# Performance work log

Measured on AMD Instinct MI355X. Metric: run time of the kernel, lower is better.

## Reference

```python
import jax, jax.numpy as jnp
import numpy as np

T, N, L = 512, 128, 256           # encoder steps, batch, decode steps
KV, VS = 128, 128                 # key_size, value_size
EMB, HID, VOC = 256, 512, 34


def _lstm_cell(x, h, c, W_ih, W_hh, b_ih, b_hh):
    # PyTorch LSTMCell gate order: i, f, g, o
    g = x @ W_ih.T + b_ih + h @ W_hh.T + b_hh
    i, f, gg, o = jnp.split(g, 4, axis=-1)
    c2 = jax.nn.sigmoid(f) * c + jax.nn.sigmoid(i) * jnp.tanh(gg)
    h2 = jax.nn.sigmoid(o) * jnp.tanh(c2)
    return h2, c2


def setup_inputs() -> dict:
    k = jax.random.key(0)
    ks = jax.random.split(k, 16)
    s = 0.05
    return {
        "key": jax.random.normal(ks[0], (T, N, KV), jnp.float32),
        "values": jax.random.normal(ks[1], (T, N, VS), jnp.float32),
        "lens": jax.random.randint(ks[2], (N,), 1, T + 1),
        "text": jax.random.randint(ks[3], (N, L), 0, VOC),
        "emb": jax.random.normal(ks[4], (VOC, EMB), jnp.float32) * s,
        "W_ih1": jax.random.normal(ks[5], (4 * HID, EMB + VS), jnp.float32) * s,
        "W_hh1": jax.random.normal(ks[6], (4 * HID, HID), jnp.float32) * s,
        "b_ih1": jnp.zeros((4 * HID,), jnp.float32),
        "b_hh1": jnp.zeros((4 * HID,), jnp.float32),
        "W_ih2": jax.random.normal(ks[7], (4 * KV, HID), jnp.float32) * s,
        "W_hh2": jax.random.normal(ks[8], (4 * KV, KV), jnp.float32) * s,
        "b_ih2": jnp.zeros((4 * KV,), jnp.float32),
        "b_hh2": jnp.zeros((4 * KV,), jnp.float32),
        "W_out": jax.random.normal(ks[9], (VOC, KV + VS), jnp.float32) * s,
        "b_out": jnp.zeros((VOC,), jnp.float32),
    }


def reference(key, values, lens, text, emb, W_ih1, W_hh1, b_ih1, b_hh1,
              W_ih2, W_hh2, b_ih2, b_hh2, W_out, b_out):
    # key/values: (T, N, 128); teacher-forced decode over L steps.
    pad_mask = jnp.arange(T)[None, :] >= lens[:, None]        # (N, T)
    embs = emb[text]                                          # (N, L, EMB)
    embs = jnp.transpose(embs, (1, 0, 2))                     # (L, N, EMB)

    def step(carry, e_t):
        h1, c1, h2, c2, ctx = carry
        x = jnp.concatenate([e_t, ctx], axis=-1)
        h1, c1 = _lstm_cell(x, h1, c1, W_ih1, W_hh1, b_ih1, b_hh1)
        h2, c2 = _lstm_cell(h1, h2, c2, W_ih2, W_hh2, b_ih2, b_hh2)
        # masked bmm attention: energy (N, T)
        energy = jnp.einsum('tnk,nk->nt', key, h2)
        energy = jnp.where(pad_mask, -1e9, energy)
        attn = jax.nn.softmax(energy, axis=1)
        ctx = jnp.einsum('nt,tnv->nv', attn, values)
        pred = jnp.concatenate([h2, ctx], axis=-1) @ W_out.T + b_out
        return (h1, c1, h2, c2, ctx), pred

    init = (jnp.zeros((N, HID)), jnp.zeros((N, HID)),
            jnp.zeros((N, KV)), jnp.zeros((N, KV)),
            jnp.zeros((N, VS)))
    _, preds = jax.lax.scan(step, init, embs)                 # (L, N, VOC)
    return jnp.transpose(preds, (1, 0, 2))                    # (N, L, VOC)
```

## Files before the change

kernel.cpp:

```cpp
#include <hip/hip_runtime.h>
#include <math.h>

#define LDEC 256
#define VOCD 34
#define SPIN_MAX 2000000u
#define XSTR 660

typedef __attribute__((ext_vector_type(8))) short bf16x8;
typedef __attribute__((ext_vector_type(8))) unsigned short u16x8;
typedef __attribute__((ext_vector_type(4))) float f32x4;

#define OFF_W1H  0u
#define OFF_W1L  2621440u
#define OFF_W2H  5242880u
#define OFF_W2L  5898240u
#define OFF_EG   6553600u
#define OFF_B2   6832128u
#define OFF_WOT  6834176u
#define OFF_H1P  6868992u
#define OFF_H2P  7393280u
#define OFF_CTXP 7524352u
#define OFF_C1   7589888u
#define OFF_C2   7852032u
#define OFF_FLG  7917568u
#define OFF_KB   7966720u
#define OFF_VB   24743936u
#define WS_NEED  41521152u

__device__ __forceinline__ float sigf(float x) { return 1.0f / (1.0f + expf(-x)); }
__device__ __forceinline__ unsigned short f2b(float x) {
  unsigned int u = __float_as_uint(x);
  unsigned int r = (u + 0x7FFFu + ((u >> 16) & 1u)) >> 16;
  return (unsigned short)r;
}
__device__ __forceinline__ float b2f(unsigned short h) {
  return __uint_as_float(((unsigned int)h) << 16);
}
__device__ __forceinline__ unsigned packf(float x) {
  unsigned short hi = f2b(x);
  unsigned short lo = f2b(x - b2f(hi));
  return ((unsigned)hi << 16) | (unsigned)lo;
}
__device__ __forceinline__ float unpackf(unsigned p) {
  return b2f((unsigned short)(p >> 16)) + b2f((unsigned short)(p & 0xffffu));
}
__device__ __forceinline__ unsigned aload(const unsigned* p) {
  return __hip_atomic_load((unsigned*)p, __ATOMIC_RELAXED, __HIP_MEMORY_SCOPE_AGENT);
}
__device__ __forceinline__ void astore(unsigned* p, unsigned v) {
  __hip_atomic_store(p, v, __ATOMIC_RELAXED, __HIP_MEMORY_SCOPE_AGENT);
}
__device__ __forceinline__ void unpack8(const unsigned* p, bf16x8& xh, bf16x8& xl) {
#pragma unroll
  for (int j = 0; j < 8; j++) {
    unsigned v = p[j];
    xh[j] = (short)(v >> 16);
    xl[j] = (short)(v & 0xffffu);
  }
}

__global__ __launch_bounds__(256) void pack_w1(const float* __restrict__ Wih1,
                                               const float* __restrict__ Whh1,
                                               unsigned short* __restrict__ W1H,
                                               unsigned short* __restrict__ W1L) {
  int idx = blockIdx.x * 256 + threadIdx.x;
  int m = idx / 640, k = idx % 640;
  int u = m >> 2, q = m & 3;
  int g = q * 512 + u;
  float v = (k < 128) ? Wih1[g * 384 + 256 + k] : Whh1[g * 512 + (k - 128)];
  unsigned short hi = f2b(v);
  W1H[idx] = hi;
  W1L[idx] = f2b(v - b2f(hi));
}

__global__ __launch_bounds__(256) void pack_w2(const float* __restrict__ Wih2,
                                               const float* __restrict__ Whh2,
                                               unsigned short* __restrict__ W2H,
                                               unsigned short* __restrict__ W2L) {
  int idx = blockIdx.x * 256 + threadIdx.x;
  int m = idx / 640, k = idx % 640;
  int u = m >> 2, q = m & 3;
  int g = q * 128 + u;
  float v = (k < 512) ? Wih2[g * 512 + k] : Whh2[g * 128 + (k - 512)];
  unsigned short hi = f2b(v);
  W2H[idx] = hi;
  W2L[idx] = f2b(v - b2f(hi));
}

__global__ __launch_bounds__(256) void pack_eg(const float* __restrict__ emb,
                                               const float* __restrict__ Wih1,
                                               const float* __restrict__ bih1,
                                               const float* __restrict__ bhh1,
                                               float* __restrict__ EG) {
  int idx = blockIdx.x * 256 + threadIdx.x;
  int v = idx >> 11, m = idx & 2047;
  int u = m >> 2, q = m & 3;
  int g = q * 512 + u;
  float acc = bih1[g] + bhh1[g];
  const float* e = emb + v * 256;
  const float* w = Wih1 + g * 384;
  for (int k = 0; k < 256; k++) acc += e[k] * w[k];
  EG[idx] = acc;
}

__global__ __launch_bounds__(256) void pack_misc(const float* __restrict__ Wout,
                                                 const float* __restrict__ bih2,
                                                 const float* __restrict__ bhh2,
                                                 float* __restrict__ WoT,
                                                 float* __restrict__ B2) {
  int idx = blockIdx.x * 256 + threadIdx.x;
  if (idx < 8704) {
    int k = idx / 34, v = idx % 34;
    WoT[idx] = Wout[v * 256 + k];
  } else if (idx < 9216) {
    int m = idx - 8704;
    int u = m >> 2, q = m & 3;
    int g = q * 128 + u;
    B2[m] = bih2[g] + bhh2[g];
  }
}

__global__ __launch_bounds__(256) void pack_kv(const float* __restrict__ key,
                                               const float* __restrict__ values,
                                               unsigned short* __restrict__ KB,
                                               unsigned short* __restrict__ VB) {
  size_t idx = (size_t)blockIdx.x * 256 + threadIdx.x;
  KB[idx] = f2b(key[idx]);
  VB[idx] = f2b(values[idx]);
}

__device__ __forceinline__ void stage_h1(int gang, int tid, int rbuf,
                                         unsigned* xshA, const unsigned* __restrict__ H1P) {
  int kcol = tid & 15, nl = (tid >> 4) & 15, rep = tid >> 8;
  int n = gang * 16 + nl;
  const unsigned* h1p = H1P + rbuf * 65536 + n * 512;
#pragma unroll
  for (int j = 0; j < 10; j++) {
    int k = rep * 160 + j * 16 + kcol;
    if (k >= 128) xshA[nl * XSTR + k] = aload(h1p + (k - 128));
  }
}
__device__ __forceinline__ void stage_ctx(int gang, int tid,
                                          unsigned* xshA, const unsigned* __restrict__ CTXP) {
  int kcol = tid & 15, nl = (tid >> 4) & 15, rep = tid >> 8;
  int n = gang * 16 + nl;
  if (rep == 0) {
#pragma unroll
    for (int j = 0; j < 8; j++) {
      int k = j * 16 + kcol;
      xshA[nl * XSTR + k] = aload(CTXP + n * 128 + k);
    }
  }
}

__device__ __forceinline__ void A_pre(
    int gidx, int tid,
    const unsigned* __restrict__ xshA,
    const unsigned short* __restrict__ W1H, const unsigned short* __restrict__ W1L,
    f32x4& p0, f32x4& p1, f32x4& p2)
{
  const int wid = tid >> 6, lane = tid & 63;
  const int l15 = lane & 15, lg = lane >> 4;
  const int gr = wid >> 2, gwid = wid & 3;
  const int kb0 = gwid * 160;
  const int mt = (gidx & 7) * 16 + (gidx >> 3) * 4 + gr;

  const unsigned short* whp = W1H + (size_t)(mt * 16 + l15) * 640 + kb0 + lg * 8;
  const unsigned short* wlp = W1L + (size_t)(mt * 16 + l15) * 640 + kb0 + lg * 8;
  const unsigned* xrow = xshA + l15 * XSTR + kb0 + lg * 8;
  f32x4 a0 = {0.0f, 0.0f, 0.0f, 0.0f};
  f32x4 a1 = {0.0f, 0.0f, 0.0f, 0.0f};
  f32x4 a2 = {0.0f, 0.0f, 0.0f, 0.0f};
  const int ks0 = (gwid == 0) ? 4 : 0;
#pragma unroll
  for (int ks = 0; ks < 5; ks++) {
    if (ks < ks0) continue;
    unsigned parr[8];
    *(uint4*)parr       = *(const uint4*)(xrow + ks * 32);
    *(uint4*)(parr + 4) = *(const uint4*)(xrow + ks * 32 + 4);
    bf16x8 xh_, xl_;
    unpack8(parr, xh_, xl_);
    bf16x8 wh_ = *(const bf16x8*)(whp + ks * 32);
    bf16x8 wl_ = *(const bf16x8*)(wlp + ks * 32);
    a0 = __builtin_amdgcn_mfma_f32_16x16x32_bf16(wh_, xh_, a0, 0, 0, 0);
    a1 = __builtin_amdgcn_mfma_f32_16x16x32_bf16(wl_, xh_, a1, 0, 0, 0);
    a2 = __builtin_amdgcn_mfma_f32_16x16x32_bf16(wh_, xl_, a2, 0, 0, 0);
  }
  p0 = a0; p1 = a1; p2 = a2;
}

__device__ __forceinline__ void A_post(
    int gang, int gidx, int tid, int t, int wp,
    const unsigned* __restrict__ xshA, float* bred,
    const unsigned short* __restrict__ W1H, const unsigned short* __restrict__ W1L,
    const float* __restrict__ EG, const int* __restrict__ text,
    unsigned* __restrict__ H1P, float* __restrict__ C1,
    f32x4 p0, f32x4 p1, f32x4 p2)
{
  const int wid = tid >> 6, lane = tid & 63;
  const int l15 = lane & 15, lg = lane >> 4;
  const int gr = wid >> 2, gwid = wid & 3;
  const int mt = (gidx & 7) * 16 + (gidx >> 3) * 4 + gr;

  if (gwid == 0) {
    const unsigned short* whp = W1H + (size_t)(mt * 16 + l15) * 640 + lg * 8;
    const unsigned short* wlp = W1L + (size_t)(mt * 16 + l15) * 640 + lg * 8;
    const unsigned* xrow = xshA + l15 * XSTR + lg * 8;
#pragma unroll
    for (int ks = 0; ks < 4; ks++) {
      unsigned parr[8];
      *(uint4*)parr       = *(const uint4*)(xrow + ks * 32);
      *(uint4*)(parr + 4) = *(const uint4*)(xrow + ks * 32 + 4);
      bf16x8 xh_, xl_;
      unpack8(parr, xh_, xl_);
      bf16x8 wh_ = *(const bf16x8*)(whp + ks * 32);
      bf16x8 wl_ = *(const bf16x8*)(wlp + ks * 32);
      p0 = __builtin_amdgcn_mfma_f32_16x16x32_bf16(wh_, xh_, p0, 0, 0, 0);
      p1 = __builtin_amdgcn_mfma_f32_16x16x32_bf16(wl_, xh_, p1, 0, 0, 0);
      p2 = __builtin_amdgcn_mfma_f32_16x16x32_bf16(wh_, xl_, p2, 0, 0, 0);
    }
  }
  f32x4 acc = p0 + p1;
  acc = acc + p2;
#pragma unroll
  for (int q = 0; q < 4; q++) bred[gr * 1024 + q * 256 + gwid * 64 + lane] = acc[q];
  __syncthreads();

  if (gwid == 0) {
    const float* br = bred + gr * 1024;
    int n = gang * 16 + l15;
    int tok = text[n * LDEC + t];
    f32x4 egv = *(const f32x4*)(EG + (size_t)tok * 2048 + mt * 16 + lg * 4);
    float g0 = br[lane]       + br[64 + lane]  + br[128 + lane] + br[192 + lane] + egv[0];
    float g1 = br[256 + lane] + br[320 + lane] + br[384 + lane] + br[448 + lane] + egv[1];
    float g2 = br[512 + lane] + br[576 + lane] + br[640 + lane] + br[704 + lane] + egv[2];
    float g3 = br[768 + lane] + br[832 + lane] + br[896 + lane] + br[960 + lane] + egv[3];
    float ig = sigf(g0), fg = sigf(g1), gg = tanhf(g2), og = sigf(g3);
    int u = mt * 4 + lg;
    float c = fg * C1[u * 128 + n] + ig * gg;
    float h = og * tanhf(c);
    C1[u * 128 + n] = c;
    astore(H1P + wp * 65536 + n * 512 + u, packf(h));
  }
  __syncthreads();
}

__device__ __forceinline__ void A_compute(
    int gang, int gidx, int tid, int t, int wp,
    const unsigned* __restrict__ xshA, float* bred,
    const unsigned short* __restrict__ W1H, const unsigned short* __restrict__ W1L,
    const float* __restrict__ EG, const int* __restrict__ text,
    unsigned* __restrict__ H1P, float* __restrict__ C1)
{
  f32x4 p0, p1, p2;
  A_pre(gidx, tid, xshA, W1H, W1L, p0, p1, p2);
  A_post(gang, gidx, tid, t, wp, xshA, bred, W1H, W1L, EG, text, H1P, C1, p0, p1, p2);
}

__device__ __forceinline__ void dev_phaseB(
    int gang, int gidx, int tid, int rp, int wp, float* bred,
    const unsigned short* __restrict__ W2H, const unsigned short* __restrict__ W2L,
    const float* __restrict__ B2,
    const unsigned* __restrict__ H1P, unsigned* __restrict__ H2P,
    float* __restrict__ C2)
{
  const int wid = tid >> 6, lane = tid & 63;
  const int l15 = lane & 15, lg = lane >> 4;
  const int mtB = (gidx & 7) * 4 + (gidx >> 3);
  if (tid < 256) {
    const int kb0 = wid * 160;
    int n = gang * 16 + l15;
    const unsigned* x1 = H1P + wp * 65536 + n * 512;
    const unsigned* x2 = H2P + rp * 16384 + n * 128;
    const unsigned short* whp = W2H + (size_t)(mtB * 16 + l15) * 640 + kb0 + lg * 8;
    const unsigned short* wlp = W2L + (size_t)(mtB * 16 + l15) * 640 + kb0 + lg * 8;
    f32x4 a0 = {0.0f, 0.0f, 0.0f, 0.0f};
    f32x4 a1 = {0.0f, 0.0f, 0.0f, 0.0f};
    f32x4 a2 = {0.0f, 0.0f, 0.0f, 0.0f};
#pragma unroll
    for (int ks = 0; ks < 5; ks++) {
      int kb = kb0 + ks * 32;
      unsigned parr[8];
      const unsigned* src = (kb < 512) ? (x1 + kb + lg * 8) : (x2 + (kb - 512) + lg * 8);
#pragma unroll
      for (int j = 0; j < 8; j++) parr[j] = aload(src + j);
      bf16x8 xh_, xl_;
      unpack8(parr, xh_, xl_);
      bf16x8 wh_ = *(const bf16x8*)(whp + ks * 32);
      bf16x8 wl_ = *(const bf16x8*)(wlp + ks * 32);
      a0 = __builtin_amdgcn_mfma_f32_16x16x32_bf16(wh_, xh_, a0, 0, 0, 0);
      a1 = __builtin_amdgcn_mfma_f32_16x16x32_bf16(wl_, xh_, a1, 0, 0, 0);
      a2 = __builtin_amdgcn_mfma_f32_16x16x32_bf16(wh_, xl_, a2, 0, 0, 0);
    }
    f32x4 acc = a0 + a1;
    acc = acc + a2;
#pragma unroll
    for (int q = 0; q < 4; q++) bred[q * 256 + wid * 64 + lane] = acc[q];
  }
  __syncthreads();
  if (tid < 64) {
    f32x4 b2v = *(const f32x4*)(B2 + mtB * 16 + lg * 4);
    float g0 = bred[lane]       + bred[64 + lane]  + bred[128 + lane] + bred[192 + lane] + b2v[0];
    float g1 = bred[256 + lane] + bred[320 + lane] + bred[384 + lane] + bred[448 + lane] + b2v[1];
    float g2 = bred[512 + lane] + bred[576 + lane] + bred[640 + lane] + bred[704 + lane] + b2v[2];
    float g3 = bred[768 + lane] + bred[832 + lane] + bred[896 + lane] + bred[960 + lane] + b2v[3];
    int n = gang * 16 + l15;
    int u = mtB * 4 + lg;
    float c = sigf(g1) * C2[u * 128 + n] + sigf(g0) * tanhf(g2);
    float h = sigf(g3) * tanhf(c);
    C2[u * 128 + n] = c;
    astore(H2P + wp * 16384 + n * 128 + u, packf(h));
  }
  __syncthreads();
}

template <int BF16KV>
__device__ __forceinline__ void dev_phaseC(
    int n, int tid, int len, int t, int wp,
    float* cred, float* es, float* h2s, float* ctxs, float* pr, float* sred,
    const float* __restrict__ key, const float* __restrict__ values,
    const unsigned short* __restrict__ KB, const unsigned short* __restrict__ VB,
    const unsigned* __restrict__ H2P, const float* __restrict__ WoT,
    const float* __restrict__ bout, unsigned* __restrict__ CTXP,
    float* __restrict__ out, unsigned* sCslot, unsigned tv)
{
  const int wid = tid >> 6, lane = tid & 63;
  if (tid < 128) h2s[tid] = unpackf(aload(H2P + wp * 16384 + n * 128 + tid));
  __syncthreads();
  float ls = 0.0f;
  if (tid < len) {
    float acc = 0.0f;
    if (BF16KV) {
      const u16x8* kr = (const u16x8*)(KB + ((size_t)tid * 128 + n) * 128);
#pragma unroll 4
      for (int k = 0; k < 16; k++) {
        u16x8 kv = kr[k];
#pragma unroll
        for (int j = 0; j < 8; j++) acc += b2f(kv[j]) * h2s[k * 8 + j];
      }
    } else {
      const float4* kr = (const float4*)(key + ((size_t)tid * 128 + n) * 128);
#pragma unroll 8
      for (int k = 0; k < 32; k++) {
        float4 kv = kr[k];
        acc += kv.x * h2s[4 * k] + kv.y * h2s[4 * k + 1] + kv.z * h2s[4 * k + 2] + kv.w * h2s[4 * k + 3];
      }
    }
    float p = expf(acc - 20.0f);
    es[tid] = p;
    ls = p;
  }
  ls += __shfl_xor(ls, 32); ls += __shfl_xor(ls, 16); ls += __shfl_xor(ls, 8);
  ls += __shfl_xor(ls, 4);  ls += __shfl_xor(ls, 2);  ls += __shfl_xor(ls, 1);
  if (lane == 0) sred[wid] = ls;
  __syncthreads();
  float S = 0.0f;
#pragma unroll
  for (int w = 0; w < 16; w++) S += sred[w];
  {
    int v4 = (tid & 31) * 4, tp = tid >> 5;
    float ax = 0.0f, ay = 0.0f, az = 0.0f, aw = 0.0f;
    if (BF16KV) {
#pragma unroll 2
      for (int tt = tp; tt < len; tt += 32) {
        float p = es[tt];
        const unsigned* w = (const unsigned*)(VB + ((size_t)tt * 128 + n) * 128 + v4);
        unsigned w0 = w[0], w1 = w[1];
        ax += p * b2f((unsigned short)(w0 & 0xffffu));
        ay += p * b2f((unsigned short)(w0 >> 16));
        az += p * b2f((unsigned short)(w1 & 0xffffu));
        aw += p * b2f((unsigned short)(w1 >> 16));
      }
    } else {
#pragma unroll 2
      for (int tt = tp; tt < len; tt += 32) {
        float p = es[tt];
        const float4 vv = *(const float4*)(values + ((size_t)tt * 128 + n) * 128 + v4);
        ax += p * vv.x; ay += p * vv.y; az += p * vv.z; aw += p * vv.w;
      }
    }
    float4 a4 = {ax, ay, az, aw};
    *(float4*)&cred[tp * 132 + v4] = a4;
  }
  __syncthreads();
  if (tid < 128) {
    float s4 = 0.0f;
#pragma unroll 8
    for (int tp2 = 0; tp2 < 32; tp2++) s4 += cred[tp2 * 132 + tid];
    float cv = s4 / S;
    ctxs[tid] = cv;
    astore(CTXP + n * 128 + tid, packf(cv));
  }
  __syncthreads();
  if (sCslot && tid == 0) astore(sCslot, tv);
  if (tid < 68) {
    int vv = tid % 34, part = tid / 34;
    const float* src = part ? ctxs : h2s;
    const float* wcol = WoT + (part ? 128 * 34 : 0);
    float a = 0.0f;
#pragma unroll 8
    for (int k2 = 0; k2 < 128; k2++) a += src[k2] * wcol[k2 * 34 + vv];
    pr[tid] = a;
  }
  __syncthreads();
  if (tid < 34) {
    out[(size_t)n * (LDEC * VOCD) + t * VOCD + tid] = bout[tid] + pr[tid] + pr[34 + tid];
  }
  __syncthreads();
}

template <int BF16KV>
__global__ void __launch_bounds__(1024, 1) decoder_coop(
    const float* __restrict__ key, const float* __restrict__ values,
    const unsigned short* __restrict__ KB, const unsigned short* __restrict__ VB,
    const int* __restrict__ lens, const int* __restrict__ text,
    const float* __restrict__ EG, const float* __restrict__ B2,
    const float* __restrict__ WoT, const float* __restrict__ bout,
    const unsigned short* __restrict__ W1H, const unsigned short* __restrict__ W1L,
    const unsigned short* __restrict__ W2H, const unsigned short* __restrict__ W2L,
    unsigned* __restrict__ CTXP, unsigned* __restrict__ H1P,
    unsigned* __restrict__ H2P, float* __restrict__ C1, float* __restrict__ C2,
    unsigned* __restrict__ FLG, float* __restrict__ out)
{
  __shared__ unsigned xshA[16 * XSTR];
  __shared__ float bred[4096];
  __shared__ float cred[4224];
  __shared__ float es[512];
  __shared__ float h2s[128];
  __shared__ float ctxs[128];
  __shared__ float pr[68];
  __shared__ float sred[16];
  __shared__ unsigned deadsh;

  const int bid = blockIdx.x, tid = threadIdx.x;
  const int gang = bid >> 5, gidx = bid & 31;
  unsigned* sA = FLG + gang * 512;
  unsigned* sB = FLG + 4096 + gang * 512;
  unsigned* sC = FLG + 8192 + gang * 256;
  const int cn = gang * 16 + gidx;
  const int clen = (gidx < 16) ? lens[cn] : 0;

  unsigned budget = SPIN_MAX;
  if (tid == 0) deadsh = 0u;

  stage_h1(gang, tid, 1, xshA, H1P);
  __syncthreads();
  f32x4 p0, p1, p2;
  A_pre(gidx, tid, xshA, W1H, W1L, p0, p1, p2);

  for (int t = 0; t < LDEC; t++) {
    const int wp = t & 1, rp = (t + 1) & 1;
    const unsigned tv = (unsigned)(t + 1);

    stage_ctx(gang, tid, xshA, CTXP);
    __syncthreads();
    A_post(gang, gidx, tid, t, wp, xshA, bred, W1H, W1L, EG, text, H1P, C1,
           p0, p1, p2);
    if (tid == 0) astore(sA + gidx * 16, tv);
    if (tid < 32) {
      unsigned* s = sA + tid * 16;
      while (aload(s) < tv) {
        if (--budget == 0) { deadsh = 1u; break; }
      }
    }
    __syncthreads();

    dev_phaseB(gang, gidx, tid, rp, wp, bred, W2H, W2L, B2, H1P, H2P, C2);
    if (tid == 0) astore(sB + gidx * 16, tv);

    stage_h1(gang, tid, wp, xshA, H1P);
    __syncthreads();
    if (t < LDEC - 1) A_pre(gidx, tid, xshA, W1H, W1L, p0, p1, p2);

    if (gidx < 16) {
      if (tid < 32) {
        unsigned* s = sB + tid * 16;
        while (aload(s) < tv) {
          if (--budget == 0) { deadsh = 1u; break; }
        }
      }
      __syncthreads();
      dev_phaseC<BF16KV>(cn, tid, clen, t, wp, cred, es, h2s, ctxs, pr, sred,
                         key, values, KB, VB, H2P, WoT, bout, CTXP, out,
                         sC + gidx * 16, tv);
    }
    if (tid < 16) {
      unsigned* s = sC + tid * 16;
      while (aload(s) < tv) {
        if (--budget == 0) { deadsh = 1u; break; }
      }
    }
    __syncthreads();
  }

  if (tid == 0 && deadsh) out[0] = 7.0e6f;
}

extern "C" void kernel_launch(void* const* d_in, const int* in_sizes, int n_in,
                              void* d_out, int out_size, void* d_ws, size_t ws_size,
                              hipStream_t stream) {
  const float* key    = (const float*)d_in[0];
  const float* values = (const float*)d_in[1];
  const int*   lens   = (const int*)d_in[2];
  const int*   text   = (const int*)d_in[3];
  const float* emb    = (const float*)d_in[4];
  const float* Wih1   = (const float*)d_in[5];
  const float* Whh1   = (const float*)d_in[6];
  const float* bih1   = (const float*)d_in[7];
  const float* bhh1   = (const float*)d_in[8];
  const float* Wih2   = (const float*)d_in[9];
  const float* Whh2   = (const float*)d_in[10];
  const float* bih2   = (const float*)d_in[11];
  const float* bhh2   = (const float*)d_in[12];
  const float* Wout   = (const float*)d_in[13];
  const float* bout   = (const float*)d_in[14];

  char* ws = (char*)d_ws;
  unsigned short* W1H = (unsigned short*)(ws + OFF_W1H);
  unsigned short* W1L = (unsigned short*)(ws + OFF_W1L);
  unsigned short* W2H = (unsigned short*)(ws + OFF_W2H);
  unsigned short* W2L = (unsigned short*)(ws + OFF_W2L);
  float* EG   = (float*)(ws + OFF_EG);
  float* B2   = (float*)(ws + OFF_B2);
  float* WoT  = (float*)(ws + OFF_WOT);
  unsigned* H1P  = (unsigned*)(ws + OFF_H1P);
  unsigned* H2P  = (unsigned*)(ws + OFF_H2P);
  unsigned* CTXP = (unsigned*)(ws + OFF_CTXP);
  float* C1   = (float*)(ws + OFF_C1);
  float* C2   = (float*)(ws + OFF_C2);
  unsigned* FLG = (unsigned*)(ws + OFF_FLG);
  unsigned short* KB = (unsigned short*)(ws + OFF_KB);
  unsigned short* VB = (unsigned short*)(ws + OFF_VB);
  float* out  = (float*)d_out;

  const bool use16 = (ws_size >= (size_t)WS_NEED);

  hipMemsetAsync(CTXP, 0, 65536, stream);
  hipMemsetAsync((char*)H1P + 262144, 0, 262144, stream);
  hipMemsetAsync((char*)H2P + 65536, 0, 65536, stream);
  hipMemsetAsync(C1,  0, 262144, stream);
  hipMemsetAsync(C2,  0, 65536, stream);
  hipMemsetAsync(FLG, 0, 49152, stream);

  pack_w1  <<<5120, 256, 0, stream>>>(Wih1, Whh1, W1H, W1L);
  pack_w2  <<<1280, 256, 0, stream>>>(Wih2, Whh2, W2H, W2L);
  pack_eg  <<<272,  256, 0, stream>>>(emb, Wih1, bih1, bhh1, EG);
  pack_misc<<<36,   256, 0, stream>>>(Wout, bih2, bhh2, WoT, B2);
  if (use16) pack_kv<<<32768, 256, 0, stream>>>(key, values, KB, VB);

  if (use16) {
    decoder_coop<1><<<256, 1024, 0, stream>>>(
        key, values, KB, VB, lens, text, EG, B2, WoT, bout,
        W1H, W1L, W2H, W2L, CTXP, H1P, H2P, C1, C2, FLG, out);
  } else {
    decoder_coop<0><<<256, 1024, 0, stream>>>(
        key, values, KB, VB, lens, text, EG, B2, WoT, bout,
        W1H, W1L, W2H, W2L, CTXP, H1P, H2P, C1, C2, FLG, out);
  }
}
```

Before: 7.997 ms.

## Compute second LSTM layer redundantly per attention block to drop a grid barrier

The second LSTM cell is no longer split across the 32 blocks of a gang with a global flag barrier and global H2/C2 buffers. Each of the 16 attention blocks now computes the full 16x128 layer-2 state for its gang, keeping h2 and c2 in shared memory and reading h1 from the already staged shared tile. This removes one cross-block spin-wait per decode step and the global round trips for h2. In exchange, the layer-2 GEMM work is duplicated 16-fold, it is serialised over 8 rounds with extra __syncthreads, and the non-attention blocks sit idle in that phase.

```diff
diff --git a/kernel.cpp b/kernel.cpp
--- a/kernel.cpp
+++ b/kernel.cpp
@@ -18,10 +18,8 @@
 #define OFF_B2   6832128u
 #define OFF_WOT  6834176u
 #define OFF_H1P  6868992u
-#define OFF_H2P  7393280u
 #define OFF_CTXP 7524352u
 #define OFF_C1   7589888u
-#define OFF_C2   7852032u
 #define OFF_FLG  7917568u
 #define OFF_KB   7966720u
 #define OFF_VB   24743936u
@@ -245,35 +243,24 @@
   __syncthreads();
 }
 
-__device__ __forceinline__ void A_compute(
-    int gang, int gidx, int tid, int t, int wp,
-    const unsigned* __restrict__ xshA, float* bred,
-    const unsigned short* __restrict__ W1H, const unsigned short* __restrict__ W1L,
-    const float* __restrict__ EG, const int* __restrict__ text,
-    unsigned* __restrict__ H1P, float* __restrict__ C1)
-{
-  f32x4 p0, p1, p2;
-  A_pre(gidx, tid, xshA, W1H, W1L, p0, p1, p2);
-  A_post(gang, gidx, tid, t, wp, xshA, bred, W1H, W1L, EG, text, H1P, C1, p0, p1, p2);
-}
-
-__device__ __forceinline__ void dev_phaseB(
-    int gang, int gidx, int tid, int rp, int wp, float* bred,
+__device__ __forceinline__ void gates2_compute(
+    int gang, int gidx, int tid, float* bred,
+    const unsigned* __restrict__ xshA,
+    unsigned* h2a_r, unsigned* h2a_w,
+    float* c2all, float* h2s,
     const unsigned short* __restrict__ W2H, const unsigned short* __restrict__ W2L,
-    const float* __restrict__ B2,
-    const unsigned* __restrict__ H1P, unsigned* __restrict__ H2P,
-    float* __restrict__ C2)
+    const float* __restrict__ B2)
 {
   const int wid = tid >> 6, lane = tid & 63;
   const int l15 = lane & 15, lg = lane >> 4;
-  const int mtB = (gidx & 7) * 4 + (gidx >> 3);
-  if (tid < 256) {
-    const int kb0 = wid * 160;
-    int n = gang * 16 + l15;
-    const unsigned* x1 = H1P + wp * 65536 + n * 512;
-    const unsigned* x2 = H2P + rp * 16384 + n * 128;
-    const unsigned short* whp = W2H + (size_t)(mtB * 16 + l15) * 640 + kb0 + lg * 8;
-    const unsigned short* wlp = W2L + (size_t)(mtB * 16 + l15) * 640 + kb0 + lg * 8;
+  const int gr = wid >> 2, gwid = wid & 3;
+  const int kb0 = gwid * 160;
+
+#pragma unroll 1
+  for (int r = 0; r < 8; r++) {
+    const int mt2 = r * 4 + gr;
+    const unsigned short* whp = W2H + (size_t)(mt2 * 16 + l15) * 640 + kb0 + lg * 8;
+    const unsigned short* wlp = W2L + (size_t)(mt2 * 16 + l15) * 640 + kb0 + lg * 8;
     f32x4 a0 = {0.0f, 0.0f, 0.0f, 0.0f};
     f32x4 a1 = {0.0f, 0.0f, 0.0f, 0.0f};
     f32x4 a2 = {0.0f, 0.0f, 0.0f, 0.0f};
@@ -281,9 +268,15 @@
     for (int ks = 0; ks < 5; ks++) {
       int kb = kb0 + ks * 32;
       unsigned parr[8];
-      const unsigned* src = (kb < 512) ? (x1 + kb + lg * 8) : (x2 + (kb - 512) + lg * 8);
-#pragma unroll
-      for (int j = 0; j < 8; j++) parr[j] = aload(src + j);
+      if (kb < 512) {
+        const unsigned* src = xshA + l15 * XSTR + 128 + kb + lg * 8;
+        *(uint4*)parr       = *(const uint4*)src;
+        *(uint4*)(parr + 4) = *(const uint4*)(src + 4);
+      } else {
+        const unsigned* src = h2a_r + l15 * 128 + (kb - 512) + lg * 8;
+        *(uint4*)parr       = *(const uint4*)src;
+        *(uint4*)(parr + 4) = *(const uint4*)(src + 4);
+      }
       bf16x8 xh_, xl_;
       unpack8(parr, xh_, xl_);
       bf16x8 wh_ = *(const bf16x8*)(whp + ks * 32);
@@ -295,38 +288,38 @@
     f32x4 acc = a0 + a1;
     acc = acc + a2;
 #pragma unroll
-    for (int q = 0; q < 4; q++) bred[q * 256 + wid * 64 + lane] = acc[q];
-  }
-  __syncthreads();
-  if (tid < 64) {
-    f32x4 b2v = *(const f32x4*)(B2 + mtB * 16 + lg * 4);
-    float g0 = bred[lane]       + bred[64 + lane]  + bred[128 + lane] + bred[192 + lane] + b2v[0];
-    float g1 = bred[256 + lane] + bred[320 + lane] + bred[384 + lane] + bred[448 + lane] + b2v[1];
-    float g2 = bred[512 + lane] + bred[576 + lane] + bred[640 + lane] + bred[704 + lane] + b2v[2];
-    float g3 = bred[768 + lane] + bred[832 + lane] + bred[896 + lane] + bred[960 + lane] + b2v[3];
-    int n = gang * 16 + l15;
-    int u = mtB * 4 + lg;
-    float c = sigf(g1) * C2[u * 128 + n] + sigf(g0) * tanhf(g2);
-    float h = sigf(g3) * tanhf(c);
-    C2[u * 128 + n] = c;
-    astore(H2P + wp * 16384 + n * 128 + u, packf(h));
-  }
-  __syncthreads();
+    for (int q = 0; q < 4; q++) bred[gr * 1024 + q * 256 + gwid * 64 + lane] = acc[q];
+    __syncthreads();
+    if (gwid == 0) {
+      const float* br = bred + gr * 1024;
+      f32x4 b2v = *(const f32x4*)(B2 + mt2 * 16 + lg * 4);
+      float g0 = br[lane]       + br[64 + lane]  + br[128 + lane] + br[192 + lane] + b2v[0];
+      float g1 = br[256 + lane] + br[320 + lane] + br[384 + lane] + br[448 + lane] + b2v[1];
+      float g2 = br[512 + lane] + br[576 + lane] + br[640 + lane] + br[704 + lane] + b2v[2];
+      float g3 = br[768 + lane] + br[832 + lane] + br[896 + lane] + br[960 + lane] + b2v[3];
+      int u = mt2 * 4 + lg;
+      int sidx = l15 * 128 + u;
+      float c = sigf(g1) * c2all[sidx] + sigf(g0) * tanhf(g2);
+      float h = sigf(g3) * tanhf(c);
+      c2all[sidx] = c;
+      h2a_w[sidx] = packf(h);
+      if (l15 == gidx) h2s[u] = h;
+    }
+    __syncthreads();
+  }
 }
 
 template <int BF16KV>
-__device__ __forceinline__ void dev_phaseC(
-    int n, int tid, int len, int t, int wp,
-    float* cred, float* es, float* h2s, float* ctxs, float* pr, float* sred,
+__device__ __forceinline__ void attn_compute(
+    int n, int tid, int len, int t,
+    float* cred, float* es, const float* h2s, float* ctxs, float* pr, float* sred,
     const float* __restrict__ key, const float* __restrict__ values,
     const unsigned short* __restrict__ KB, const unsigned short* __restrict__ VB,
-    const unsigned* __restrict__ H2P, const float* __restrict__ WoT,
-    const float* __restrict__ bout, unsigned* __restrict__ CTXP,
-    float* __restrict__ out, unsigned* sCslot, unsigned tv)
+    const float* __restrict__ WoT, const float* __restrict__ bout,
+    unsigned* __restrict__ CTXP, float* __restrict__ out,
+    unsigned* sCslot, unsigned tv)
 {
   const int wid = tid >> 6, lane = tid & 63;
-  if (tid < 128) h2s[tid] = unpackf(aload(H2P + wp * 16384 + n * 128 + tid));
-  __syncthreads();
   float ls = 0.0f;
   if (tid < len) {
     float acc = 0.0f;
@@ -392,7 +385,7 @@
     astore(CTXP + n * 128 + tid, packf(cv));
   }
   __syncthreads();
-  if (sCslot && tid == 0) astore(sCslot, tv);
+  if (tid == 0) astore(sCslot, tv);
   if (tid < 68) {
     int vv = tid % 34, part = tid / 34;
     const float* src = part ? ctxs : h2s;
@@ -419,8 +412,7 @@
     const unsigned short* __restrict__ W1H, const unsigned short* __restrict__ W1L,
     const unsigned short* __restrict__ W2H, const unsigned short* __restrict__ W2L,
     unsigned* __restrict__ CTXP, unsigned* __restrict__ H1P,
-    unsigned* __restrict__ H2P, float* __restrict__ C1, float* __restrict__ C2,
-    unsigned* __restrict__ FLG, float* __restrict__ out)
+    float* __restrict__ C1, unsigned* __restrict__ FLG, float* __restrict__ out)
 {
   __shared__ unsigned xshA[16 * XSTR];
   __shared__ float bred[4096];
@@ -430,18 +422,21 @@
   __shared__ float ctxs[128];
   __shared__ float pr[68];
   __shared__ float sred[16];
+  __shared__ unsigned h2a[2][2048];
+  __shared__ float c2all[2048];
   __shared__ unsigned deadsh;
 
   const int bid = blockIdx.x, tid = threadIdx.x;
   const int gang = bid >> 5, gidx = bid & 31;
   unsigned* sA = FLG + gang * 512;
-  unsigned* sB = FLG + 4096 + gang * 512;
   unsigned* sC = FLG + 8192 + gang * 256;
   const int cn = gang * 16 + gidx;
   const int clen = (gidx < 16) ? lens[cn] : 0;
 
   unsigned budget = SPIN_MAX;
   if (tid == 0) deadsh = 0u;
+
+  for (int i = tid; i < 2048; i += 1024) { h2a[1][i] = 0u; c2all[i] = 0.0f; }
 
   stage_h1(gang, tid, 1, xshA, H1P);
   __syncthreads();
@@ -465,25 +460,20 @@
     }
     __syncthreads();
 
-    dev_phaseB(gang, gidx, tid, rp, wp, bred, W2H, W2L, B2, H1P, H2P, C2);
-    if (tid == 0) astore(sB + gidx * 16, tv);
-
     stage_h1(gang, tid, wp, xshA, H1P);
     __syncthreads();
-    if (t < LDEC - 1) A_pre(gidx, tid, xshA, W1H, W1L, p0, p1, p2);
 
     if (gidx < 16) {
-      if (tid < 32) {
-        unsigned* s = sB + tid * 16;
-        while (aload(s) < tv) {
-          if (--budget == 0) { deadsh = 1u; break; }
-        }
-      }
-      __syncthreads();
-      dev_phaseC<BF16KV>(cn, tid, clen, t, wp, cred, es, h2s, ctxs, pr, sred,
-                         key, values, KB, VB, H2P, WoT, bout, CTXP, out,
-                         sC + gidx * 16, tv);
-    }
+      gates2_compute(gang, gidx, tid, bred, xshA, h2a[rp], h2a[wp], c2all, h2s,
+                     W2H, W2L, B2);
+      attn_compute<BF16KV>(cn, tid, clen, t, cred, es, h2s, ctxs, pr, sred,
+                           key, values, KB, VB, WoT, bout, CTXP, out,
+                           sC + gidx * 16, tv);
+      A_pre(gidx, tid, xshA, W1H, W1L, p0, p1, p2);
+    } else {
+      A_pre(gidx, tid, xshA, W1H, W1L, p0, p1, p2);
+    }
+
     if (tid < 16) {
       unsigned* s = sC + tid * 16;
       while (aload(s) < tv) {
@@ -524,10 +514,8 @@
   float* B2   = (float*)(ws + OFF_B2);
   float* WoT  = (float*)(ws + OFF_WOT);
   unsigned* H1P  = (unsigned*)(ws + OFF_H1P);
-  unsigned* H2P  = (unsigned*)(ws + OFF_H2P);
   unsigned* CTXP = (unsigned*)(ws + OFF_CTXP);
   float* C1   = (float*)(ws + OFF_C1);
-  float* C2   = (float*)(ws + OFF_C2);
   unsigned* FLG = (unsigned*)(ws + OFF_FLG);
   unsigned short* KB = (unsigned short*)(ws + OFF_KB);
   unsigned short* VB = (unsigned short*)(ws + OFF_VB);
@@ -537,9 +525,7 @@
 
   hipMemsetAsync(CTXP, 0, 65536, stream);
   hipMemsetAsync((char*)H1P + 262144, 0, 262144, stream);
-  hipMemsetAsync((char*)H2P + 65536, 0, 65536, stream);
   hipMemsetAsync(C1,  0, 262144, stream);
-  hipMemsetAsync(C2,  0, 65536, stream);
   hipMemsetAsync(FLG, 0, 49152, stream);
 
   pack_w1  <<<5120, 256, 0, stream>>>(Wih1, Whh1, W1H, W1L);
@@ -551,10 +537,10 @@
   if (use16) {
     decoder_coop<1><<<256, 1024, 0, stream>>>(
         key, values, KB, VB, lens, text, EG, B2, WoT, bout,
-        W1H, W1L, W2H, W2L, CTXP, H1P, H2P, C1, C2, FLG, out);
+        W1H, W1L, W2H, W2L, CTXP, H1P, C1, FLG, out);
   } else {
     decoder_coop<0><<<256, 1024, 0, stream>>>(
         key, values, KB, VB, lens, text, EG, B2, WoT, bout,
-        W1H, W1L, W2H, W2L, CTXP, H1P, H2P, C1, C2, FLG, out);
-  }
-}
+        W1H, W1L, W2H, W2L, CTXP, H1P, C1, FLG, out);
+  }
+}
```

Result: slower. 17.57 ms (+119.7%).
